# Kernel optimization log

Hardware: AMD Instinct MI355X
Metric: run time of the kernel (lower is better)

Reference implementation:

```python
import jax, jax.numpy as jnp
import numpy as np

B, L, D, H, C = 16, 512, 1280, 512, 5


def setup_inputs() -> dict:
    key = jax.random.key(0)
    ks = jax.random.split(key, 20)
    emb = jax.random.normal(ks[0], (B, L, D), jnp.float32)
    lengths = jax.random.randint(ks[1], (B,), 16, L + 1)
    attention_mask = (jnp.arange(L)[None, :] < lengths[:, None]).astype(jnp.int32)
    sc = 1.0 / np.sqrt(H)
    u = lambda k, s: jax.random.uniform(k, s, jnp.float32, -sc, sc)
    return dict(
        embeddings=emb,
        attention_mask=attention_mask,
        h0=jax.random.normal(ks[2], (2, B, H), jnp.float32),
        c0=jax.random.normal(ks[3], (2, B, H), jnp.float32),
        w_ih_f=u(ks[4], (4 * H, D)), w_hh_f=u(ks[5], (4 * H, H)),
        b_ih_f=u(ks[6], (4 * H,)), b_hh_f=u(ks[7], (4 * H,)),
        w_ih_b=u(ks[8], (4 * H, D)), w_hh_b=u(ks[9], (4 * H, H)),
        b_ih_b=u(ks[10], (4 * H,)), b_hh_b=u(ks[11], (4 * H,)),
        w_out=u(ks[12], (2 * H, C)), b_out=u(ks[13], (C,)),
        crf_start=jax.random.normal(ks[14], (C,), jnp.float32) * 0.1,
        crf_end=jax.random.normal(ks[15], (C,), jnp.float32) * 0.1,
        crf_trans=jax.random.normal(ks[16], (C, C), jnp.float32) * 0.1,
    )


def _lstm_dir(x, h0, c0, w_ih, w_hh, b_ih, b_hh):
    # x: [B, T, D] -> hidden states [B, T, H]; PyTorch gate order (i, f, g, o)
    xg = jnp.einsum('btd,gd->btg', x, w_ih) + b_ih + b_hh  # [B, T, 4H]

    def step(carry, xw_t):
        h, c = carry
        g = xw_t + h @ w_hh.T
        i, f, gg, o = jnp.split(g, 4, axis=-1)
        c = jax.nn.sigmoid(f) * c + jax.nn.sigmoid(i) * jnp.tanh(gg)
        h = jax.nn.sigmoid(o) * jnp.tanh(c)
        return (h, c), h

    _, hs = jax.lax.scan(step, (h0, c0), xg.transpose(1, 0, 2))
    return hs.transpose(1, 0, 2)


def _emissions(embeddings, attention_mask, h0, c0, w_ih_f, w_hh_f, b_ih_f, b_hh_f,
               w_ih_b, w_hh_b, b_ih_b, b_hh_b, w_out, b_out):
    lengths = attention_mask.sum(axis=1)
    x = embeddings[:, 1:-1]                                   # drop CLS position, shift left
    Tp = x.shape[1]
    valid = jnp.arange(Tp)[None, :] < (lengths - 2)[:, None]  # remove_cls crop [1:len-1], left-aligned pad
    x = jnp.where(valid[:, :, None], x, 0.0)
    hf = _lstm_dir(x, h0[0], c0[0], w_ih_f, w_hh_f, b_ih_f, b_hh_f)
    hb = _lstm_dir(x[:, ::-1], h0[1], c0[1], w_ih_b, w_hh_b, b_ih_b, b_hh_b)[:, ::-1]
    h = jnp.concatenate([hf, hb], axis=-1)                    # [B, Tp, 2H]
    return h @ w_out + b_out, valid


def _viterbi_decode(emissions, mask, start, end, trans):
    Bn, Tp, Ct = emissions.shape
    ident = jnp.arange(Ct, dtype=jnp.int32)
    score0 = start[None, :] + emissions[:, 0]                 # [B, C]

    def step(score, inp):
        emit_t, m_t = inp                                      # [B, C], [B]
        br = score[:, :, None] + trans[None] + emit_t[:, None, :]
        ns = br.max(axis=1)
        idx = br.argmax(axis=1).astype(jnp.int32)
        idx = jnp.where(m_t[:, None], idx, ident[None, :])     # identity backpointer past seq end
        score = jnp.where(m_t[:, None], ns, score)
        return score, idx

    score, hist = jax.lax.scan(step, score0,
                               (emissions[:, 1:].transpose(1, 0, 2), mask[:, 1:].T))
    score = score + end[None, :]
    last = jnp.argmax(score, axis=-1).astype(jnp.int32)        # [B]
    bidx = jnp.arange(Bn)

    def bstep(tag, idx_t):
        prev = idx_t[bidx, tag]
        return prev, prev

    _, prevs = jax.lax.scan(bstep, last, hist, reverse=True)   # [Tp-1, B]
    tags = jnp.concatenate([prevs, last[None, :]], axis=0).transpose(1, 0)
    return tags


def reference(embeddings, attention_mask, h0, c0, w_ih_f, w_hh_f, b_ih_f, b_hh_f,
              w_ih_b, w_hh_b, b_ih_b, b_hh_b, w_out, b_out, crf_start, crf_end, crf_trans):
    emissions, valid = _emissions(embeddings, attention_mask, h0, c0,
                                  w_ih_f, w_hh_f, b_ih_f, b_hh_f,
                                  w_ih_b, w_hh_b, b_ih_b, b_hh_b, w_out, b_out)
    tags = _viterbi_decode(emissions, valid, crf_start, crf_end, crf_trans)
    return tags, valid  # tags valid where mask True (past-end entries repeat last tag)
```

## Files before the change

### kernel.cpp

```cpp
#include <hip/hip_runtime.h>

typedef unsigned short u16;
typedef unsigned int u32;
typedef __bf16 bf16x8 __attribute__((ext_vector_type(8)));
typedef u16 u16x8 __attribute__((ext_vector_type(8)));
typedef float f32x4 __attribute__((ext_vector_type(4)));
typedef u32 u32x4 __attribute__((ext_vector_type(4)));

#define B_ 16
#define T_ 510
#define H_ 512
#define N_ 4096
#define KSPLIT 2560

#define OFF_ABIG  0ull
#define OFF_BBIG  41943040ull
#define OFF_BIAS  62914560ull
#define OFF_XG    62930944ull
#define OFF_HS    197148672ull
#define OFF_EMIS  230572032ull
#define OFF_V     230735232ull
#define OFF_FLAGS 230735296ull
#define OFF_HBUF  230735552ull
#define OFF_HBUFB  (OFF_EMIS)
#define OFF_FLAGSB (OFF_EMIS + 131072ull)
#define OFF_PROBE  (OFF_EMIS + 131328ull)
#define OFF_CTRL   (OFF_EMIS + 131584ull)
#define OFF_PROBE2 (OFF_EMIS + 131648ull)

#define MAGIC_  0x5EC0FFEE
#define MAGIC2_ 0x7A57C0DE
#define MAGIC3_ 0x3C0DE777
#define POLL_BUDGET 65536
#define PHB_BUDGET  8192
#define ARB_BUDGET  262144

#define GL_LDS(g, s) __builtin_amdgcn_global_load_lds(                      \
    (const __attribute__((address_space(1))) void*)(g),                     \
    (__attribute__((address_space(3))) void*)(s), 16, 0, 0)

__device__ __forceinline__ u16 f2bf(float x) {
  u32 u = __float_as_uint(x);
  u32 r = (u + 0x7fffu + ((u >> 16) & 1u)) >> 16;
  return (u16)r;
}
__device__ __forceinline__ float bf2f(u16 h) { return __uint_as_float(((u32)h) << 16); }

__device__ __forceinline__ int ld_cc(const int* p) {
  int f;
  asm volatile("global_load_dword %0, %1, off sc0 sc1\n\ts_waitcnt vmcnt(0)" : "=v"(f) : "v"(p) : "memory");
  return f;
}
__device__ __forceinline__ int ld_se(const int* p) {
  int f;
  asm volatile("global_load_dword %0, %1, off sc0\n\ts_waitcnt vmcnt(0)" : "=v"(f) : "v"(p) : "memory");
  return f;
}
__device__ __forceinline__ void st_cc(int* p, int v) {
  asm volatile("global_store_dword %0, %1, off sc0 sc1\n\ts_waitcnt vmcnt(0)" :: "v"(p), "v"(v) : "memory");
}
__device__ __forceinline__ void st_plain(int* p, int v) {
  asm volatile("global_store_dword %0, %1, off\n\ts_waitcnt vmcnt(0)" :: "v"(p), "v"(v) : "memory");
}

__global__ __launch_bounds__(256) void k_prep(const int* __restrict__ mask, int* __restrict__ V,
                                              int* __restrict__ flagsA, int* __restrict__ flagsB,
                                              int* __restrict__ probe, int* __restrict__ probe2,
                                              int* __restrict__ ctrl) {
  __shared__ int red[4];
  int b = blockIdx.x, tid = threadIdx.x;
  int s = mask[b * 512 + tid] + mask[b * 512 + 256 + tid];
  for (int off = 32; off; off >>= 1) s += __shfl_down(s, off);
  if ((tid & 63) == 0) red[tid >> 6] = s;
  __syncthreads();
  if (tid == 0) V[b] = red[0] + red[1] + red[2] + red[3] - 2;
  if (b == 0 && tid < 64) flagsA[tid] = 0;
  if (b == 2 && tid < 64) flagsB[tid] = 0;
  if (b == 3 && tid < 64) probe[tid] = 0;
  if (b == 4 && tid < 64) probe2[tid] = 0;
  if (b == 1 && tid < 16) ctrl[tid] = 0;
}

__global__ __launch_bounds__(256) void k_valid(const int* __restrict__ V, int* __restrict__ out) {
  int idx = blockIdx.x * 256 + threadIdx.x;
  if (idx < B_ * T_) {
    int b = idx / T_, t = idx - b * T_;
    out[B_ * T_ + idx] = (t < V[b]) ? 1 : 0;
  }
}

__global__ __launch_bounds__(320) void k_splitA(const float* __restrict__ emb, const int* __restrict__ V,
                                                u16* __restrict__ Abig) {
  int row = blockIdx.x;
  int k0 = threadIdx.x * 4;
  u16* dst = Abig + (size_t)row * KSPLIT;
  float4 v = {0.f, 0.f, 0.f, 0.f};
  if (row < B_ * T_) {
    int b = row / T_, t = row - b * T_;
    if (t < V[b]) v = *(const float4*)(emb + (size_t)(b * 512 + t + 1) * 1280 + k0);
  }
  float vs[4] = {v.x, v.y, v.z, v.w};
  ushort4 hi, lo;
  u16 h0_ = f2bf(vs[0]); u16 l0_ = f2bf(vs[0] - bf2f(h0_));
  u16 h1_ = f2bf(vs[1]); u16 l1_ = f2bf(vs[1] - bf2f(h1_));
  u16 h2_ = f2bf(vs[2]); u16 l2_ = f2bf(vs[2] - bf2f(h2_));
  u16 h3_ = f2bf(vs[3]); u16 l3_ = f2bf(vs[3] - bf2f(h3_));
  hi.x = h0_; hi.y = h1_; hi.z = h2_; hi.w = h3_;
  lo.x = l0_; lo.y = l1_; lo.z = l2_; lo.w = l3_;
  *(ushort4*)(dst + k0) = hi;
  *(ushort4*)(dst + 1280 + k0) = lo;
}

__global__ __launch_bounds__(320) void k_splitB(const float* __restrict__ wf, const float* __restrict__ wb,
                                                const float* __restrict__ bihf, const float* __restrict__ bhhf,
                                                const float* __restrict__ bihb, const float* __restrict__ bhhb,
                                                u16* __restrict__ Bbig, float* __restrict__ bias) {
  int n = blockIdx.x;
  int k0 = threadIdx.x * 4;
  int d = n >> 11, g = n & 2047;
  const float* w = (d ? wb : wf) + (size_t)g * 1280;
  float4 v = *(const float4*)(w + k0);
  float vs[4] = {v.x, v.y, v.z, v.w};
  ushort4 hi, lo;
  u16 h0_ = f2bf(vs[0]); u16 l0_ = f2bf(vs[0] - bf2f(h0_));
  u16 h1_ = f2bf(vs[1]); u16 l1_ = f2bf(vs[1] - bf2f(h1_));
  u16 h2_ = f2bf(vs[2]); u16 l2_ = f2bf(vs[2] - bf2f(h2_));
  u16 h3_ = f2bf(vs[3]); u16 l3_ = f2bf(vs[3] - bf2f(h3_));
  hi.x = h0_; hi.y = h1_; hi.z = h2_; hi.w = h3_;
  lo.x = l0_; lo.y = l1_; lo.z = l2_; lo.w = l3_;
  u16* dst = Bbig + (size_t)n * KSPLIT;
  *(ushort4*)(dst + k0) = hi;
  *(ushort4*)(dst + 1280 + k0) = lo;
  if (threadIdx.x == 0) bias[n] = d ? (bihb[g] + bhhb[g]) : (bihf[g] + bhhf[g]);
}

__global__ __launch_bounds__(256, 2) void k_gemm(const u16* __restrict__ A, const u16* __restrict__ Bt,
                                                 const float* __restrict__ bias, float* __restrict__ C) {
  __shared__ __align__(16) u16 As[128 * 64];
  __shared__ __align__(16) u16 Bs[128 * 64];
  const int tid = threadIdx.x;
  const int w = tid >> 6, l = tid & 63;
  const int wm = w >> 1, wn = w & 1;
  const int bm = blockIdx.x, bn = blockIdx.y;
  f32x4 acc[4][4];
#pragma unroll
  for (int m = 0; m < 4; ++m)
#pragma unroll
    for (int n = 0; n < 4; ++n) acc[m][n] = (f32x4){0.f, 0.f, 0.f, 0.f};

  const int rQ = tid >> 3;
  const int cB = (tid & 7) * 16;
  const char* gA = (const char*)(A + (size_t)(bm * 128) * KSPLIT) + cB;
  const char* gB = (const char*)(Bt + (size_t)(bn * 128) * KSPLIT) + cB;

  for (int kt = 0; kt < 60; ++kt) {
    const int s = kt / 20, ks = kt - s * 20;
    const int aOff = ((s == 2) ? 1280 : 0) + ks * 64;
    const int bOff = ((s == 1) ? 1280 : 0) + ks * 64;
    __syncthreads();
#pragma unroll
    for (int q = 0; q < 4; ++q) {
      GL_LDS(gA + ((size_t)(q * 32 + rQ) * KSPLIT + aOff) * 2, (char*)As + q * 4096 + tid * 16);
      GL_LDS(gB + ((size_t)(q * 32 + rQ) * KSPLIT + bOff) * 2, (char*)Bs + q * 4096 + tid * 16);
    }
    __syncthreads();
#pragma unroll
    for (int kc = 0; kc < 2; ++kc) {
      bf16x8 af[4], bfr[4];
      const int kByte = kc * 64 + (l >> 4) * 16;
#pragma unroll
      for (int m = 0; m < 4; ++m)
        af[m] = *(const bf16x8*)((const char*)As + (wm * 64 + m * 16 + (l & 15)) * 128 + kByte);
#pragma unroll
      for (int n = 0; n < 4; ++n)
        bfr[n] = *(const bf16x8*)((const char*)Bs + (wn * 64 + n * 16 + (l & 15)) * 128 + kByte);
#pragma unroll
      for (int m = 0; m < 4; ++m)
#pragma unroll
        for (int n = 0; n < 4; ++n)
          acc[m][n] = __builtin_amdgcn_mfma_f32_16x16x32_bf16(af[m], bfr[n], acc[m][n], 0, 0, 0);
    }
  }
#pragma unroll
  for (int n = 0; n < 4; ++n) {
    const int gc = bn * 128 + wn * 64 + n * 16 + (l & 15);
    const float bv = bias[gc];
#pragma unroll
    for (int m = 0; m < 4; ++m) {
      const int gr0 = bm * 128 + wm * 64 + m * 16 + (l >> 4) * 4;
#pragma unroll
      for (int r = 0; r < 4; ++r) C[(size_t)(gr0 + r) * N_ + gc] = acc[m][n][r] + bv;
    }
  }
}

template <int COH>
__device__ void run_recur(int dir, int sub, const float* __restrict__ xg, const float* __restrict__ whh,
                          const float* __restrict__ h0, const float* __restrict__ c0,
                          float* __restrict__ hs, u16* __restrict__ hbuf, int* __restrict__ flags,
                          u16* lds_a, float* epil, float* hsh) {
  const int tid = threadIdx.x;
  const int w = tid >> 6, l = tid & 63;
  const int c = l & 15, kg = l >> 4;
  const int gate = c >> 2, uloc = c & 3;
  const int ug = sub * 16 + w * 4 + uloc;
  constexpr int GB = (COH != 0) ? 9 : 0;

  __syncthreads();

  bf16x8 whi[16], wlo[16];
  {
    const float* wrow = whh + (size_t)(gate * 512 + ug) * 512 + kg * 8;
#pragma unroll
    for (int kc = 0; kc < 16; ++kc) {
      float4 v0 = *(const float4*)(wrow + kc * 32);
      float4 v1 = *(const float4*)(wrow + kc * 32 + 4);
      float vs[8] = {v0.x, v0.y, v0.z, v0.w, v1.x, v1.y, v1.z, v1.w};
      u16x8 hi, lo;
#pragma unroll
      for (int j = 0; j < 8; ++j) {
        u16 h = f2bf(vs[j]);
        hi[j] = h;
        lo[j] = f2bf(vs[j] - bf2f(h));
      }
      whi[kc] = __builtin_bit_cast(bf16x8, hi);
      wlo[kc] = __builtin_bit_cast(bf16x8, lo);
    }
  }

  const int eb = l & 15, eu = l >> 4;
  const int eug = sub * 16 + w * 4 + eu;
  float creg = c0[(dir * 16 + eb) * 512 + eug];
  {
    float h = h0[(dir * 16 + eb) * 512 + eug];
    u16 hh = f2bf(h), hl = f2bf(h - bf2f(hh));
    size_t base = (size_t)(dir * 2) * 8192;
    u16* p0 = hbuf + base + eb * 512 + eug;
    u16* p1 = hbuf + base + 8192 + eb * 512 + eug;
    if constexpr (COH != 0) {
      asm volatile("global_store_short %0, %1, off\n\tglobal_store_short %2, %3, off\n\ts_waitcnt vmcnt(0)"
                   :: "v"(p0), "v"((u32)hh), "v"(p1), "v"((u32)hl) : "memory");
    } else {
      asm volatile("global_store_short %0, %1, off sc0 sc1\n\tglobal_store_short %2, %3, off sc0 sc1\n\ts_waitcnt vmcnt(0)"
                   :: "v"(p0), "v"((u32)hh), "v"(p1), "v"((u32)hl) : "memory");
    }
  }
  __syncthreads();
  if (tid == 0) {
    if constexpr (COH != 0) st_plain(flags + dir * 32 + sub, 1 + GB);
    else st_cc(flags + dir * 32 + sub, 1 + GB);
  }

  for (int t = 0; t < T_; ++t) {
    const int trow = dir ? (T_ - 1 - t) : t;
    f32x4 acc0;
    {
      const int n = dir * 2048 + gate * 512 + ug;
#pragma unroll
      for (int r = 0; r < 4; ++r) acc0[r] = xg[(size_t)((kg * 4 + r) * T_ + trow) * N_ + n];
    }
    if (w == 0) {
      const int* fp = flags + (dir << 5) + (l & 31);
      int it = 0;
      while (true) {
        int f;
        if constexpr (COH == 2) {
          ++it;
          if ((it & 255) == 0)
            asm volatile("global_load_dword %0, %1, off sc0 sc1\n\ts_waitcnt vmcnt(0)" : "=v"(f) : "v"(fp) : "memory");
          else
            asm volatile("global_load_dword %0, %1, off sc0\n\ts_waitcnt vmcnt(0)" : "=v"(f) : "v"(fp) : "memory");
        } else {
          asm volatile("global_load_dword %0, %1, off sc0 sc1\n\ts_waitcnt vmcnt(0)" : "=v"(f) : "v"(fp) : "memory");
        }
        if (__all(f >= t + 1 + GB)) break;
        if constexpr (COH == 0) __builtin_amdgcn_s_sleep(1);
      }
    }
    __syncthreads();

    {
      const u16* src = hbuf + (size_t)(((t & 1) * 2 + dir) * 2) * 8192;
      u32x4 v[8];
#pragma unroll
      for (int q = 0; q < 8; ++q) {
        const char* p = (const char*)src + q * 4096 + tid * 16;
        if constexpr (COH == 2)
          asm volatile("global_load_dwordx4 %0, %1, off sc0" : "=v"(v[q]) : "v"(p) : "memory");
        else
          asm volatile("global_load_dwordx4 %0, %1, off sc0 sc1" : "=v"(v[q]) : "v"(p) : "memory");
      }
      asm volatile("s_waitcnt vmcnt(0)" ::: "memory");
      __builtin_amdgcn_sched_barrier(0);
#pragma unroll
      for (int q = 0; q < 8; ++q) {
        int off = q * 4096 + tid * 16;
        int var = off >> 14;
        int rem = off & 16383;
        int b = rem >> 10;
        int inrow = rem & 1023;
        *(u32x4*)((char*)lds_a + var * 16384 + b * 1024 + (inrow ^ ((b & 7) << 4))) = v[q];
      }
    }
    __syncthreads();

    f32x4 acc1 = (f32x4){0.f, 0.f, 0.f, 0.f};
    f32x4 acc2 = (f32x4){0.f, 0.f, 0.f, 0.f};
    f32x4 acc3 = (f32x4){0.f, 0.f, 0.f, 0.f};
    f32x4 acc4 = (f32x4){0.f, 0.f, 0.f, 0.f};
    f32x4 acc5 = (f32x4){0.f, 0.f, 0.f, 0.f};
#pragma unroll
    for (int kc = 0; kc < 16; ++kc) {
      const int rowb = l & 15;
      const int koff = (kc * 64 + kg * 16) ^ ((rowb & 7) << 4);
      bf16x8 ahi = *(const bf16x8*)((const char*)lds_a + rowb * 1024 + koff);
      bf16x8 alo = *(const bf16x8*)((const char*)lds_a + 16384 + rowb * 1024 + koff);
      if (kc & 1) {
        acc3 = __builtin_amdgcn_mfma_f32_16x16x32_bf16(ahi, whi[kc], acc3, 0, 0, 0);
        acc4 = __builtin_amdgcn_mfma_f32_16x16x32_bf16(ahi, wlo[kc], acc4, 0, 0, 0);
        acc5 = __builtin_amdgcn_mfma_f32_16x16x32_bf16(alo, whi[kc], acc5, 0, 0, 0);
      } else {
        acc0 = __builtin_amdgcn_mfma_f32_16x16x32_bf16(ahi, whi[kc], acc0, 0, 0, 0);
        acc1 = __builtin_amdgcn_mfma_f32_16x16x32_bf16(ahi, wlo[kc], acc1, 0, 0, 0);
        acc2 = __builtin_amdgcn_mfma_f32_16x16x32_bf16(alo, whi[kc], acc2, 0, 0, 0);
      }
    }
    f32x4 acc = ((acc0 + acc3) + (acc1 + acc4)) + (acc2 + acc5);

#pragma unroll
    for (int r = 0; r < 4; ++r) epil[(w * 16 + kg * 4 + r) * 17 + c] = acc[r];
    asm volatile("s_waitcnt lgkmcnt(0)" ::: "memory");
    __builtin_amdgcn_sched_barrier(0);
    const float gi = epil[(w * 16 + eb) * 17 + 0 + eu];
    const float gf = epil[(w * 16 + eb) * 17 + 4 + eu];
    const float gg = epil[(w * 16 + eb) * 17 + 8 + eu];
    const float go = epil[(w * 16 + eb) * 17 + 12 + eu];
    const float si = 1.f / (1.f + __expf(-gi));
    const float sf = 1.f / (1.f + __expf(-gf));
    const float so = 1.f / (1.f + __expf(-go));
    const float tg = tanhf(gg);
    creg = sf * creg + si * tg;
    const float h = so * tanhf(creg);
    hsh[eb * 17 + w * 4 + eu] = h;
    __syncthreads();
    const int sb = tid >> 4, su = tid & 15;
    const float hv = hsh[sb * 17 + su];
    {
      u16 hh = f2bf(hv), hl = f2bf(hv - bf2f(hh));
      size_t base = (size_t)((((t + 1) & 1) * 2 + dir) * 2) * 8192;
      u16* p0 = hbuf + base + sb * 512 + sub * 16 + su;
      if constexpr (COH != 0) {
        asm volatile("global_store_short %0, %1, off\n\tglobal_store_short %2, %3, off\n\ts_waitcnt vmcnt(0)"
                     :: "v"(p0), "v"((u32)hh), "v"(p0 + 8192), "v"((u32)hl) : "memory");
      } else {
        asm volatile("global_store_short %0, %1, off sc0 sc1\n\tglobal_store_short %2, %3, off sc0 sc1\n\ts_waitcnt vmcnt(0)"
                     :: "v"(p0), "v"((u32)hh), "v"(p0 + 8192), "v"((u32)hl) : "memory");
      }
    }
    __syncthreads();
    if (tid == 0) {
      if constexpr (COH != 0) st_plain(flags + dir * 32 + sub, t + 2 + GB);
      else st_cc(flags + dir * 32 + sub, t + 2 + GB);
    }
    hs[(size_t)((dir * 16 + sb) * T_ + trow) * 512 + sub * 16 + su] = hv;
  }
}

__global__ __launch_bounds__(256, 1) void k_recur(const float* __restrict__ xg, const float* __restrict__ whh_f,
                                                  const float* __restrict__ whh_b, const float* __restrict__ h0,
                                                  const float* __restrict__ c0, float* __restrict__ hs,
                                                  u16* __restrict__ hbufA, u16* __restrict__ hbufB,
                                                  int* __restrict__ flagsA, int* __restrict__ flagsB,
                                                  int* __restrict__ probe, int* __restrict__ probe2,
                                                  int* __restrict__ ctrl) {
  __shared__ __align__(16) u16 lds_a[16384];
  __shared__ float epil[4 * 16 * 17];
  __shared__ float hsh[16 * 17];
  __shared__ int s_act, s_cfg;

  const int tid = threadIdx.x;

  if (tid == 0) {
    int xcc;
    asm volatile("s_getreg_b32 %0, hwreg(HW_REG_XCC_ID)" : "=s"(xcc));
    xcc &= 7;
    int slot = 99;
    if (xcc < 2) slot = __hip_atomic_fetch_add(&ctrl[4 + xcc], 1, __ATOMIC_RELAXED, __HIP_MEMORY_SCOPE_AGENT);
    const int roleA = (xcc < 2 && slot < 32);
    const int dir = xcc, sub = slot;
    if (roleA) {
      int* myflag = flagsA + dir * 32 + sub;
      const int fb = dir * 32;
      int mg = MAGIC_;
      asm volatile("global_store_dword %0, %1, off\n\ts_waitcnt vmcnt(0)" :: "v"(probe + fb + sub), "v"(mg) : "memory");
      st_cc(myflag, 2);
      bool complete = false;
      for (int it = 0; it < POLL_BUDGET && !complete; ++it) {
        complete = true;
        for (int j = 0; j < 32; ++j)
          if (ld_cc(flagsA + fb + j) < 2) { complete = false; break; }
        if (!complete) __builtin_amdgcn_s_sleep(16);
      }
      bool Aok = complete;
      if (Aok)
        for (int j = 0; j < 32; ++j)
          if (ld_cc(probe + fb + j) != MAGIC_) { Aok = false; break; }
      if (Aok) {
        int m2 = MAGIC2_;
        asm volatile("global_store_dword %0, %1, off\n\ts_waitcnt vmcnt(0)" :: "v"(probe2 + fb + sub), "v"(m2) : "memory");
      }
      st_cc(myflag, Aok ? 3 : 7);
      bool any7 = !Aok, arrived = false;
      for (int it = 0; it < PHB_BUDGET && !arrived && !any7; ++it) {
        arrived = true;
        for (int j = 0; j < 32; ++j) {
          int f = ld_cc(flagsA + fb + j);
          if (f == 7) { any7 = true; break; }
          if (f < 3) { arrived = false; break; }
        }
        if (!arrived && !any7) __builtin_amdgcn_s_sleep(4);
      }
      if (Aok && arrived && !any7) {
        bool r1 = true;
        for (int j = 0; j < 32; ++j)
          if (ld_se(probe2 + fb + j) != MAGIC2_) { r1 = false; break; }
        st_cc(myflag, r1 ? 4 : 8);
        if (r1) {
          bool all4 = false, any8 = false;
          for (int it = 0; it < PHB_BUDGET && !all4 && !any8; ++it) {
            all4 = true;
            for (int j = 0; j < 32; ++j) {
              int f = ld_cc(flagsA + fb + j);
              if (f == 8) { any8 = true; break; }
              if (f < 4) { all4 = false; break; }
            }
            if (!all4 && !any8) __builtin_amdgcn_s_sleep(4);
          }
          if (all4 && !any8) {
            int m3 = MAGIC3_;
            asm volatile("global_store_dword %0, %1, off\n\ts_waitcnt vmcnt(0)" :: "v"(probe2 + fb + sub), "v"(m3) : "memory");
            st_cc(myflag, 5);
            bool all5 = false;
            for (int it = 0; it < PHB_BUDGET && !all5; ++it) {
              all5 = true;
              for (int j = 0; j < 32; ++j)
                if (ld_cc(flagsA + fb + j) < 5) { all5 = false; break; }
              if (!all5) __builtin_amdgcn_s_sleep(4);
            }
            bool r2 = all5;
            if (r2)
              for (int j = 0; j < 32; ++j)
                if (ld_se(probe2 + fb + j) != MAGIC3_) { r2 = false; break; }
            st_cc(myflag, r2 ? 6 : 8);
          }
        }
      }
      if (sub == 0) {
        int verdict = Aok ? 1 : 2;
        for (int it = 0; it < PHB_BUDGET; ++it) {
          int n6 = 0;
          bool bad7 = false, bad8 = false, pending = false;
          for (int j = 0; j < 32; ++j) {
            int f = ld_cc(flagsA + fb + j);
            if (f == 7) { bad7 = true; break; }
            if (f == 8) { bad8 = true; break; }
            if (f == 6) ++n6;
            else pending = true;
          }
          if (bad7) { verdict = 2; break; }
          if (bad8) { verdict = Aok ? 1 : 2; break; }
          if (n6 == 32) { verdict = 3; break; }
          if (pending) __builtin_amdgcn_s_sleep(4);
        }
        st_cc(&ctrl[12 + dir], verdict);
      }
    }

    if (blockIdx.x == 0) {
      int v0 = 0, v1 = 0;
      for (int it = 0; it < ARB_BUDGET; ++it) {
        v0 = ld_cc(&ctrl[12]);
        v1 = ld_cc(&ctrl[13]);
        if (v0 && v1) break;
        __builtin_amdgcn_s_sleep(16);
      }
      if (!v0) v0 = 2;
      if (!v1) v1 = 2;
      st_cc(&ctrl[14], 0x100 | v0 | (v1 << 4));
    }

    int cfg;
    do {
      cfg = ld_cc(&ctrl[14]);
      if (!cfg) __builtin_amdgcn_s_sleep(16);
    } while (!cfg);

    s_cfg = cfg;
    int md = (cfg >> (dir * 4)) & 15;
    s_act = (roleA && md != 2) ? (dir | (sub << 1) | (md << 6)) : -1;
  }
  __syncthreads();
  const int act = s_act, cfg = s_cfg;

  if (act >= 0) {
    const int adir = act & 1, asub = (act >> 1) & 31, md = act >> 6;
    if (md == 3)
      run_recur<2>(adir, asub, xg, adir ? whh_b : whh_f, h0, c0, hs, hbufA, flagsA, lds_a, epil, hsh);
    else
      run_recur<1>(adir, asub, xg, adir ? whh_b : whh_f, h0, c0, hs, hbufA, flagsA, lds_a, epil, hsh);
  }
  if (blockIdx.x < 64) {
    const int mdir = (int)blockIdx.x >> 5, msub = (int)blockIdx.x & 31;
    if (((cfg >> (mdir * 4)) & 15) == 2)
      run_recur<0>(mdir, msub, xg, mdir ? whh_b : whh_f, h0, c0, hs, hbufB, flagsB, lds_a, epil, hsh);
  }
}

__global__ __launch_bounds__(256) void k_emis(const float* __restrict__ hs, const float* __restrict__ wout,
                                              const float* __restrict__ bout, float* __restrict__ e) {
  const int tid = threadIdx.x;
  const int w = tid >> 6, l = tid & 63;
  const int row = blockIdx.x * 4 + w;
  const int b = row / T_, t = row - b * T_;
  const float* hf = hs + (size_t)(b * T_ + t) * 512;
  const float* hb = hs + (size_t)((16 + b) * T_ + t) * 512;
  float a0 = 0, a1 = 0, a2 = 0, a3 = 0, a4 = 0;
#pragma unroll
  for (int it = 0; it < 8; ++it) {
    int u = it * 64 + l;
    float hv = hf[u];
    const float* wr = wout + u * 5;
    a0 += hv * wr[0]; a1 += hv * wr[1]; a2 += hv * wr[2]; a3 += hv * wr[3]; a4 += hv * wr[4];
  }
#pragma unroll
  for (int it = 0; it < 8; ++it) {
    int u = it * 64 + l;
    float hv = hb[u];
    const float* wr = wout + (512 + u) * 5;
    a0 += hv * wr[0]; a1 += hv * wr[1]; a2 += hv * wr[2]; a3 += hv * wr[3]; a4 += hv * wr[4];
  }
  for (int off = 32; off; off >>= 1) {
    a0 += __shfl_down(a0, off);
    a1 += __shfl_down(a1, off);
    a2 += __shfl_down(a2, off);
    a3 += __shfl_down(a3, off);
    a4 += __shfl_down(a4, off);
  }
  if (l == 0) {
    float* ep = e + (size_t)row * 5;
    ep[0] = a0 + bout[0];
    ep[1] = a1 + bout[1];
    ep[2] = a2 + bout[2];
    ep[3] = a3 + bout[3];
    ep[4] = a4 + bout[4];
  }
}

__global__ __launch_bounds__(64) void k_viterbi(const float* __restrict__ e, const int* __restrict__ V,
                                                const float* __restrict__ start, const float* __restrict__ endv,
                                                const float* __restrict__ trans, int* __restrict__ out) {
  __shared__ float els[T_ * 5];
  __shared__ unsigned char hist[(T_ - 1) * 5];
  __shared__ float strans[25];
  const int b = blockIdx.x, l = threadIdx.x;
  for (int i = l; i < T_ * 5; i += 64) els[i] = e[(size_t)b * T_ * 5 + i];
  if (l < 25) strans[l] = trans[l];
  const int Vb = V[b];
  __syncthreads();
  const int cl = (l < 5) ? l : 0;
  float score = (l < 5) ? (start[l] + els[l]) : -1e30f;
  for (int t = 1; t < T_; ++t) {
    const bool valid = t < Vb;
    float m = -1e30f;
    int arg = 0;
#pragma unroll
    for (int p = 0; p < 5; ++p) {
      float v = __shfl(score, p) + strans[p * 5 + cl];
      if (v > m) { m = v; arg = p; }
    }
    if (l < 5) {
      if (valid) {
        score = m + els[t * 5 + l];
        hist[(t - 1) * 5 + l] = (unsigned char)arg;
      } else {
        hist[(t - 1) * 5 + l] = (unsigned char)l;
      }
    }
  }
  float sc = (l < 5) ? (score + endv[l]) : -1e30f;
  int last = 0;
  float mb = -1e30f;
#pragma unroll
  for (int p = 0; p < 5; ++p) {
    float v = __shfl(sc, p);
    if (v > mb) { mb = v; last = p; }
  }
  __syncthreads();
  if (l == 0) {
    int tag = last;
    out[b * T_ + (T_ - 1)] = tag;
    for (int t = T_ - 2; t >= 0; --t) {
      tag = hist[t * 5 + tag];
      out[b * T_ + t] = tag;
    }
  }
}

extern "C" void kernel_launch(void* const* d_in, const int* in_sizes, int n_in, void* d_out, int out_size,
                              void* d_ws, size_t ws_size, hipStream_t stream) {
  const float* emb = (const float*)d_in[0];
  const int* amask = (const int*)d_in[1];
  const float* h0 = (const float*)d_in[2];
  const float* c0 = (const float*)d_in[3];
  const float* wihf = (const float*)d_in[4];
  const float* whhf = (const float*)d_in[5];
  const float* bihf = (const float*)d_in[6];
  const float* bhhf = (const float*)d_in[7];
  const float* wihb = (const float*)d_in[8];
  const float* whhb = (const float*)d_in[9];
  const float* bihb = (const float*)d_in[10];
  const float* bhhb = (const float*)d_in[11];
  const float* wout = (const float*)d_in[12];
  const float* bout = (const float*)d_in[13];
  const float* cstart = (const float*)d_in[14];
  const float* cend = (const float*)d_in[15];
  const float* ctrans = (const float*)d_in[16];

  char* ws = (char*)d_ws;
  u16* Abig = (u16*)(ws + OFF_ABIG);
  u16* Bbig = (u16*)(ws + OFF_BBIG);
  float* bias = (float*)(ws + OFF_BIAS);
  float* xg = (float*)(ws + OFF_XG);
  float* hs = (float*)(ws + OFF_HS);
  float* emis = (float*)(ws + OFF_EMIS);
  int* V = (int*)(ws + OFF_V);
  int* flagsA = (int*)(ws + OFF_FLAGS);
  u16* hbufA = (u16*)(ws + OFF_HBUF);
  u16* hbufB = (u16*)(ws + OFF_HBUFB);
  int* flagsB = (int*)(ws + OFF_FLAGSB);
  int* probe = (int*)(ws + OFF_PROBE);
  int* probe2 = (int*)(ws + OFF_PROBE2);
  int* ctrl = (int*)(ws + OFF_CTRL);
  int* out = (int*)d_out;

  hipLaunchKernelGGL(k_prep, dim3(16), dim3(256), 0, stream, amask, V, flagsA, flagsB, probe, probe2, ctrl);
  hipLaunchKernelGGL(k_valid, dim3(32), dim3(256), 0, stream, V, out);
  hipLaunchKernelGGL(k_splitA, dim3(8192), dim3(320), 0, stream, emb, V, Abig);
  hipLaunchKernelGGL(k_splitB, dim3(4096), dim3(320), 0, stream, wihf, wihb, bihf, bhhf, bihb, bhhb, Bbig, bias);
  hipLaunchKernelGGL(k_gemm, dim3(64, 32), dim3(256), 0, stream, Abig, Bbig, bias, xg);
  hipLaunchKernelGGL(k_recur, dim3(256), dim3(256), 0, stream, xg, whhf, whhb, h0, c0, hs, hbufA, hbufB,
                     flagsA, flagsB, probe, probe2, ctrl);
  hipLaunchKernelGGL(k_emis, dim3(2040), dim3(256), 0, stream, hs, wout, bout, emis);
  hipLaunchKernelGGL(k_viterbi, dim3(16), dim3(64), 0, stream, emis, V, cstart, cend, ctrans, out);
}
```

Before: 1.634 ms.

## Prefetch next-step input gates, add them in the epilogue, and use fast activations

The per-step xg load moves out of the MFMA accumulator initialisation. The values each thread needs for the next step are now prefetched during the current step and added to the gate pre-activations after the LDS reduction, which takes the global load latency off the critical path of the serial recurrence. Sigmoid and tanh are replaced by exp plus hardware reciprocal approximations, and the epilogue LDS stride changes from 17 to 20. The inline-asm loads have no explicit wait before use, and the fast tanh formula may lose accuracy or overflow for large inputs.

```diff
diff --git a/kernel.cpp b/kernel.cpp
--- a/kernel.cpp
+++ b/kernel.cpp
@@ -61,6 +61,15 @@
 }
 __device__ __forceinline__ void st_plain(int* p, int v) {
   asm volatile("global_store_dword %0, %1, off\n\ts_waitcnt vmcnt(0)" :: "v"(p), "v"(v) : "memory");
+}
+
+__device__ __forceinline__ float sigm_f(float x) {
+  float e = __expf(-x);
+  return __builtin_amdgcn_rcpf(1.f + e);
+}
+__device__ __forceinline__ float tanh_f(float x) {
+  float e = __expf(2.f * x);
+  return 1.f - 2.f * __builtin_amdgcn_rcpf(e + 1.f);
 }
 
 __global__ __launch_bounds__(256) void k_prep(const int* __restrict__ mask, int* __restrict__ V,
@@ -251,14 +260,18 @@
     else st_cc(flags + dir * 32 + sub, 1 + GB);
   }
 
+  float xv[4];
+  {
+    const int tr0 = dir ? (T_ - 1) : 0;
+#pragma unroll
+    for (int g = 0; g < 4; ++g) {
+      const float* p = xg + (size_t)(eb * T_ + tr0) * N_ + dir * 2048 + g * 512 + eug;
+      asm volatile("global_load_dword %0, %1, off" : "=v"(xv[g]) : "v"(p) : "memory");
+    }
+  }
+
   for (int t = 0; t < T_; ++t) {
     const int trow = dir ? (T_ - 1 - t) : t;
-    f32x4 acc0;
-    {
-      const int n = dir * 2048 + gate * 512 + ug;
-#pragma unroll
-      for (int r = 0; r < 4; ++r) acc0[r] = xg[(size_t)((kg * 4 + r) * T_ + trow) * N_ + n];
-    }
     if (w == 0) {
       const int* fp = flags + (dir << 5) + (l & 31);
       int it = 0;
@@ -304,11 +317,8 @@
     }
     __syncthreads();
 
-    f32x4 acc1 = (f32x4){0.f, 0.f, 0.f, 0.f};
-    f32x4 acc2 = (f32x4){0.f, 0.f, 0.f, 0.f};
-    f32x4 acc3 = (f32x4){0.f, 0.f, 0.f, 0.f};
-    f32x4 acc4 = (f32x4){0.f, 0.f, 0.f, 0.f};
-    f32x4 acc5 = (f32x4){0.f, 0.f, 0.f, 0.f};
+    f32x4 acc0 = (f32x4){0.f, 0.f, 0.f, 0.f};
+    f32x4 acc1 = acc0, acc2 = acc0, acc3 = acc0, acc4 = acc0, acc5 = acc0;
 #pragma unroll
     for (int kc = 0; kc < 16; ++kc) {
       const int rowb = l & 15;
@@ -328,19 +338,19 @@
     f32x4 acc = ((acc0 + acc3) + (acc1 + acc4)) + (acc2 + acc5);
 
 #pragma unroll
-    for (int r = 0; r < 4; ++r) epil[(w * 16 + kg * 4 + r) * 17 + c] = acc[r];
+    for (int r = 0; r < 4; ++r) epil[(w * 16 + kg * 4 + r) * 20 + c] = acc[r];
     asm volatile("s_waitcnt lgkmcnt(0)" ::: "memory");
     __builtin_amdgcn_sched_barrier(0);
-    const float gi = epil[(w * 16 + eb) * 17 + 0 + eu];
-    const float gf = epil[(w * 16 + eb) * 17 + 4 + eu];
-    const float gg = epil[(w * 16 + eb) * 17 + 8 + eu];
-    const float go = epil[(w * 16 + eb) * 17 + 12 + eu];
-    const float si = 1.f / (1.f + __expf(-gi));
-    const float sf = 1.f / (1.f + __expf(-gf));
-    const float so = 1.f / (1.f + __expf(-go));
-    const float tg = tanhf(gg);
+    const float gi = epil[(w * 16 + eb) * 20 + 0 + eu] + xv[0];
+    const float gf = epil[(w * 16 + eb) * 20 + 4 + eu] + xv[1];
+    const float gg = epil[(w * 16 + eb) * 20 + 8 + eu] + xv[2];
+    const float go = epil[(w * 16 + eb) * 20 + 12 + eu] + xv[3];
+    const float si = sigm_f(gi);
+    const float sf = sigm_f(gf);
+    const float so = sigm_f(go);
+    const float tg = tanh_f(gg);
     creg = sf * creg + si * tg;
-    const float h = so * tanhf(creg);
+    const float h = so * tanh_f(creg);
     hsh[eb * 17 + w * 4 + eu] = h;
     __syncthreads();
     const int sb = tid >> 4, su = tid & 15;
@@ -357,6 +367,15 @@
                      :: "v"(p0), "v"((u32)hh), "v"(p0 + 8192), "v"((u32)hl) : "memory");
       }
     }
+    {
+      const int tn = (t + 1 < T_) ? (t + 1) : t;
+      const int trn = dir ? (T_ - 1 - tn) : tn;
+#pragma unroll
+      for (int g = 0; g < 4; ++g) {
+        const float* p = xg + (size_t)(eb * T_ + trn) * N_ + dir * 2048 + g * 512 + eug;
+        asm volatile("global_load_dword %0, %1, off" : "=v"(xv[g]) : "v"(p) : "memory");
+      }
+    }
     __syncthreads();
     if (tid == 0) {
       if constexpr (COH != 0) st_plain(flags + dir * 32 + sub, t + 2 + GB);
@@ -374,7 +393,7 @@
                                                   int* __restrict__ probe, int* __restrict__ probe2,
                                                   int* __restrict__ ctrl) {
   __shared__ __align__(16) u16 lds_a[16384];
-  __shared__ float epil[4 * 16 * 17];
+  __shared__ float epil[4 * 16 * 20];
   __shared__ float hsh[16 * 17];
   __shared__ int s_act, s_cfg;
 
```

After: 1.855 ms. +13.5%, slower.
